# Optimization experiments

Measured on AMD Instinct MI355X. Metric: run time of the kernel, lower is better.

## Reference

```python
import jax, jax.numpy as jnp
import numpy as np

TAU = 2.0      # spikingjelly LIFNode default tau
V_TH = 1.0     # default v_threshold
ALPHA = 4.0    # default surrogate.Sigmoid alpha
H, HL = 8, 2   # num_heads, local_heads

@jax.custom_vjp
def spike(u):
    # Heaviside: fire when membrane potential >= threshold (u = v - v_th)
    return (u >= 0.0).astype(u.dtype)

def _spike_fwd(u):
    return spike(u), u

def _spike_bwd(u, g):
    s = jax.nn.sigmoid(ALPHA * u)
    return (g * ALPHA * s * (1.0 - s),)

spike.defvjp(_spike_fwd, _spike_bwd)

def lif(x):
    # Multi-step LIF, decay_input=False, v_reset=0.0 (hard reset), detach_reset=True.
    # Charge: v = v - (v - 0)/tau + x ; spike when v >= v_th ; reset v -> 0 where spiked.
    decay = 1.0 - 1.0 / TAU
    def step(v, xt):
        v = v * decay + xt
        s = spike(v - V_TH)
        v = v * (1.0 - jax.lax.stop_gradient(s))  # detach_reset
        return v, s
    _, spikes = jax.lax.scan(step, jnp.zeros_like(x[0]), x)
    return spikes

def setup_inputs() -> dict:
    key = jax.random.key(0)
    ks = jax.random.split(key, 5)
    T, B, C, D = 4, 8, 512, 768
    hd = D // H            # 96
    mkv = hd * HL          # 192 (GQA kv projection width)
    scale = 0.1            # keeps LIF membrane potentials near threshold
    return {
        "x": jax.random.normal(ks[0], (T, B, C, D), jnp.float32),
        "q_w": jax.random.normal(ks[1], (D, D), jnp.float32) * scale,
        "k_w": jax.random.normal(ks[2], (mkv, D), jnp.float32) * scale,
        "v_w": jax.random.normal(ks[3], (mkv, D), jnp.float32) * scale,
        "wo_w": jax.random.normal(ks[4], (D, D), jnp.float32) * scale,
    }

def reference(x, q_w, k_w, v_w, wo_w):
    T, B, C, D = x.shape
    hd = D // H
    n_rep = H // HL
    xs = lif(x)  # proj_lif
    # q: (T,B,C,D) -> (T,B,H,C,hd)
    q = lif(xs @ q_w.T).reshape(T, B, C, H, hd).transpose(0, 1, 3, 2, 4)
    # k,v: (T,B,C,mkv) -> repeat_interleave over kv heads -> (T,B,H,C,hd)
    k = lif(xs @ k_w.T).reshape(T, B, C, HL, hd)
    k = jnp.repeat(k, n_rep, axis=3).transpose(0, 1, 3, 2, 4)
    v = lif(xs @ v_w.T).reshape(T, B, C, HL, hd)
    v = jnp.repeat(v, n_rep, axis=3).transpose(0, 1, 3, 2, 4)
    # softmax-free attention: (q k^T) * 0.1 @ v
    scores = jnp.einsum('tbhqd,tbhkd->tbhqk', q, k) * 0.1
    out = jnp.einsum('tbhqk,tbhkd->tbhqd', scores, v)
    # (T,B,H,C,hd) -> (T,B,C,D)
    out = out.transpose(0, 1, 3, 2, 4).reshape(T, B, C, D)
    return out @ wo_w.T
```

## Files before the change

kernel.cpp:

```cpp
#include <hip/hip_runtime.h>

typedef __bf16 bf16;
typedef __bf16 bf16x8 __attribute__((ext_vector_type(8)));
typedef float f32x4 __attribute__((ext_vector_type(4)));

#define T_ 4
#define B_ 8
#define C_ 512
#define D_ 768
#define H_ 8
#define HL_ 2
#define HD_ 96
#define MKV_ 192
#define M2_ 4096
#define BCD_ 3145728
#define M3_ 16384
#define NCOMB 1152
#define SUSP_CAP 65536
#define SUSP_WIN 2e-4f

__device__ __forceinline__ void gld16(const bf16* g, bf16* l) {
    __builtin_amdgcn_global_load_lds(
        (const __attribute__((address_space(1))) unsigned int*)g,
        (__attribute__((address_space(3))) unsigned int*)l, 16, 0, 0);
}

__global__ __launch_bounds__(256) void prep_kernel(
    const float* __restrict__ x, const float* __restrict__ q_w,
    const float* __restrict__ k_w, const float* __restrict__ v_w,
    const float* __restrict__ wo_w, bf16* __restrict__ xs,
    bf16* __restrict__ whi, bf16* __restrict__ wlo, bf16* __restrict__ wo_bf,
    unsigned* __restrict__ susp)
{
    const int t0 = blockIdx.x * 256 + threadIdx.x;
    const int stride = gridDim.x * 256;
    if (t0 == 0) susp[0] = 0;
    for (int i = t0; i < BCD_; i += stride) {
        double v = 0.0;
        #pragma unroll
        for (int t = 0; t < T_; ++t) {
            v = v * 0.5 + (double)x[(size_t)t * BCD_ + i];
            float s = (v >= 1.0) ? 1.0f : 0.0f;
            xs[(size_t)t * BCD_ + i] = (bf16)s;
            if (s != 0.0f) v = 0.0;
        }
    }
    for (int i = t0; i < NCOMB * D_; i += stride) {
        int row = i / D_, col = i - row * D_;
        float v;
        if (row < 768)      v = q_w[(size_t)row * D_ + col];
        else if (row < 960) v = k_w[(size_t)(row - 768) * D_ + col];
        else                v = v_w[(size_t)(row - 960) * D_ + col];
        bf16 h = (bf16)v;
        whi[i] = h;
        wlo[i] = (bf16)(v - (float)h);
    }
    for (int i = t0; i < D_ * D_; i += stride)
        wo_bf[i] = (bf16)wo_w[i];
}

__global__ __launch_bounds__(256) void proj_lif_kernel(
    const bf16* __restrict__ xs, const bf16* __restrict__ Whi,
    const bf16* __restrict__ Wlo,
    bf16* __restrict__ q_sp, bf16* __restrict__ k_sp, bf16* __restrict__ v_sp,
    unsigned* __restrict__ susp)
{
    __shared__ __align__(16) bf16 Alds[T_][64 * 64];
    __shared__ __align__(16) bf16 Hlds[64 * 64];
    __shared__ __align__(16) bf16 Llds[64 * 64];

    const int tid  = threadIdx.x;
    const int wave = tid >> 6, lane = tid & 63;
    const int m16  = lane & 15, quad = lane >> 4;
    const int wm   = wave >> 1, wn = wave & 1;
    const int m0   = blockIdx.x * 64;
    const int n0   = blockIdx.y * 64;

    const int colb = n0 + wn * 32;
    bf16* outp; int Nloc, cb;
    if (colb < 768)      { outp = q_sp; Nloc = 768; cb = colb; }
    else if (colb < 960) { outp = k_sp; Nloc = 192; cb = colb - 768; }
    else                 { outp = v_sp; Nloc = 192; cb = colb - 960; }

    f32x4 acc[T_][2][2];
    #pragma unroll
    for (int t = 0; t < T_; t++)
        #pragma unroll
        for (int a = 0; a < 2; a++)
            #pragma unroll
            for (int b = 0; b < 2; b++) { f32x4 z = {0.f,0.f,0.f,0.f}; acc[t][a][b] = z; }

    for (int k0 = 0; k0 < D_; k0 += 64) {
        __syncthreads();
        #pragma unroll
        for (int j = 0; j < 8; j++) {
            int ci = j * 256 + tid;
            int t = ci >> 9, rem = ci & 511, row = rem >> 3, slot = rem & 7;
            int seg = slot ^ ((row >> 1) & 7);
            gld16(xs + (size_t)(t * M2_ + m0 + row) * D_ + k0 + seg * 8, &Alds[t][rem * 8]);
        }
        #pragma unroll
        for (int j = 0; j < 2; j++) {
            int ci = j * 256 + tid;
            int row = ci >> 3, slot = ci & 7;
            int seg = slot ^ ((row >> 1) & 7);
            gld16(Whi + (size_t)(n0 + row) * D_ + k0 + seg * 8, Hlds + ci * 8);
            gld16(Wlo + (size_t)(n0 + row) * D_ + k0 + seg * 8, Llds + ci * 8);
        }
        __syncthreads();

        #pragma unroll
        for (int kc = 0; kc < 2; kc++) {
            bf16x8 a[T_][2], bh[2], bl[2];
            #pragma unroll
            for (int mi = 0; mi < 2; mi++) {
                int row = wm * 32 + mi * 16 + m16;
                int off = row * 64 + (((kc * 4 + quad) ^ ((row >> 1) & 7)) * 8);
                #pragma unroll
                for (int t = 0; t < T_; t++)
                    a[t][mi] = *(const bf16x8*)&Alds[t][off];
            }
            #pragma unroll
            for (int ni = 0; ni < 2; ni++) {
                int row = wn * 32 + ni * 16 + m16;
                int off = row * 64 + (((kc * 4 + quad) ^ ((row >> 1) & 7)) * 8);
                bh[ni] = *(const bf16x8*)&Hlds[off];
                bl[ni] = *(const bf16x8*)&Llds[off];
            }
            #pragma unroll
            for (int ni = 0; ni < 2; ni++)
                #pragma unroll
                for (int t = 0; t < T_; t++)
                    #pragma unroll
                    for (int mi = 0; mi < 2; mi++) {
                        acc[t][mi][ni] = __builtin_amdgcn_mfma_f32_16x16x32_bf16(a[t][mi], bh[ni], acc[t][mi][ni], 0, 0, 0);
                        acc[t][mi][ni] = __builtin_amdgcn_mfma_f32_16x16x32_bf16(a[t][mi], bl[ni], acc[t][mi][ni], 0, 0, 0);
                    }
        }
    }

    #pragma unroll
    for (int mi = 0; mi < 2; mi++)
        #pragma unroll
        for (int ni = 0; ni < 2; ni++)
            #pragma unroll
            for (int rr = 0; rr < 4; rr++) {
                int row = m0 + wm * 32 + mi * 16 + quad * 4 + rr;
                int lc  = cb + ni * 16 + m16;
                float v = 0.f;
                bool suspect = false;
                #pragma unroll
                for (int t = 0; t < T_; t++) {
                    v = v * 0.5f + acc[t][mi][ni][rr];
                    float d = v - 1.0f;
                    if (fabsf(d) < SUSP_WIN) suspect = true;
                    float sp = (d >= 0.f) ? 1.f : 0.f;
                    v *= (1.f - sp);
                    outp[(size_t)(t * M2_ + row) * Nloc + lc] = (bf16)sp;
                }
                if (suspect) {
                    int ccol = n0 + wn * 32 + ni * 16 + m16;
                    unsigned idx = atomicAdd(susp, 1u);
                    if (idx < SUSP_CAP) susp[1 + idx] = (unsigned)(row * 2048 + ccol);
                }
            }
}

__global__ __launch_bounds__(256) void fixup_kernel(
    const bf16* __restrict__ xs, const float* __restrict__ q_w,
    const float* __restrict__ k_w, const float* __restrict__ v_w,
    bf16* __restrict__ q_sp, bf16* __restrict__ k_sp, bf16* __restrict__ v_sp,
    const unsigned* __restrict__ susp)
{
    unsigned count = susp[0];
    if (count > SUSP_CAP) count = SUSP_CAP;
    const int lane = threadIdx.x & 63;
    const int wid  = (blockIdx.x * blockDim.x + threadIdx.x) >> 6;
    const int nw   = (gridDim.x * blockDim.x) >> 6;
    for (unsigned i = wid; i < count; i += nw) {
        unsigned e = susp[1 + i];
        int row = e >> 11, col = e & 2047;
        const float* W; bf16* outp; int Nloc, lc;
        if (col < 768)      { W = q_w + (size_t)col * D_;         outp = q_sp; Nloc = 768; lc = col; }
        else if (col < 960) { W = k_w + (size_t)(col - 768) * D_; outp = k_sp; Nloc = 192; lc = col - 768; }
        else                { W = v_w + (size_t)(col - 960) * D_; outp = v_sp; Nloc = 192; lc = col - 960; }
        double v = 0.0;
        for (int t = 0; t < T_; ++t) {
            const bf16* ar = xs + (size_t)(t * M2_ + row) * D_;
            double y = 0.0;
            for (int k = lane; k < D_; k += 64)
                y += (double)(float)ar[k] * (double)W[k];
            #pragma unroll
            for (int off = 1; off < 64; off <<= 1)
                y += __shfl_xor(y, off);
            v = v * 0.5 + y;
            unsigned sp = (v >= 1.0) ? 1u : 0u;
            if (lane == 0) outp[(size_t)(t * M2_ + row) * Nloc + lc] = (bf16)(float)sp;
            if (sp) v = 0.0;
        }
    }
}

__global__ __launch_bounds__(256) void ktv_kernel(
    const bf16* __restrict__ k_sp, const bf16* __restrict__ v_sp,
    float* __restrict__ M_part)
{
    const int g    = blockIdx.x;
    const int cc   = blockIdx.y;
    const int kvh  = g % HL_;
    const int tb   = g / HL_;
    const int wave = threadIdx.x >> 6;
    const int lane = threadIdx.x & 63;
    const int m16  = lane & 15, quad = lane >> 4;

    __shared__ __align__(16) bf16 klds[96 * 40];
    __shared__ __align__(16) bf16 vlds[96 * 40];

    f32x4 acc[9];
    #pragma unroll
    for (int i = 0; i < 9; i++) { f32x4 z = {0.f,0.f,0.f,0.f}; acc[i] = z; }

    const bf16* kbase = k_sp + ((size_t)tb * C_ + cc * 128) * MKV_ + kvh * HD_;
    const bf16* vbase = v_sp + ((size_t)tb * C_ + cc * 128) * MKV_ + kvh * HD_;

    for (int c0 = 0; c0 < 128; c0 += 32) {
        __syncthreads();
        for (int idx = threadIdx.x; idx < 32 * 96; idx += 256) {
            int d = idx % 96;
            int c = idx / 96;
            klds[d * 40 + c] = kbase[(size_t)(c0 + c) * MKV_ + d];
            vlds[d * 40 + c] = vbase[(size_t)(c0 + c) * MKV_ + d];
        }
        __syncthreads();
        #pragma unroll
        for (int i = 0; i < 9; i++) {
            int tile = wave + i * 4;
            int mt = tile / 6, nt = tile % 6;
            bf16x8 a = *(const bf16x8*)(&klds[(mt * 16 + m16) * 40 + quad * 8]);
            bf16x8 b = *(const bf16x8*)(&vlds[(nt * 16 + m16) * 40 + quad * 8]);
            acc[i] = __builtin_amdgcn_mfma_f32_16x16x32_bf16(a, b, acc[i], 0, 0, 0);
        }
    }
    float* op = M_part + ((size_t)cc * 64 + g) * HD_ * HD_;
    #pragma unroll
    for (int i = 0; i < 9; i++) {
        int tile = wave + i * 4;
        int mt = tile / 6, nt = tile % 6;
        #pragma unroll
        for (int r = 0; r < 4; r++) {
            int d = mt * 16 + quad * 4 + r;
            int j = nt * 16 + m16;
            op[(size_t)j * HD_ + d] = acc[i][r];
        }
    }
}

__global__ __launch_bounds__(256) void cvtM_kernel(
    const float* __restrict__ M_part, bf16* __restrict__ M_hi,
    bf16* __restrict__ M_lo)
{
    int i = blockIdx.x * 256 + threadIdx.x;
    if (i >= 64 * HD_ * HD_) return;
    float m = M_part[i] + M_part[i + 589824] + M_part[i + 2 * 589824] + M_part[i + 3 * 589824];
    bf16 h = (bf16)m;
    M_hi[i] = h;
    M_lo[i] = (bf16)(m - (float)h);
}

__global__ __launch_bounds__(256) void qm_kernel(
    const bf16* __restrict__ q_sp, const bf16* __restrict__ M_hi,
    const bf16* __restrict__ M_lo, bf16* __restrict__ out_attn)
{
    const int tbh  = blockIdx.x;
    const int h    = tbh % H_;
    const int tb   = tbh / H_;
    const int g    = tb * HL_ + (h >> 2);
    const int wave = threadIdx.x >> 6;
    const int lane = threadIdx.x & 63;
    const int m16  = lane & 15, quad = lane >> 4;
    const int cw   = blockIdx.y * 128 + wave * 32;

    __shared__ __align__(16) bf16 Mh[96 * 104];
    __shared__ __align__(16) bf16 Ml[96 * 104];
    {
        const bf16* gh = M_hi + (size_t)g * HD_ * HD_;
        const bf16* gl = M_lo + (size_t)g * HD_ * HD_;
        #pragma unroll
        for (int j = 0; j < 5; j++) {
            int ci = j * 256 + threadIdx.x;
            if (ci < 1152) {
                int row = ci / 12, seg = ci % 12;
                *(bf16x8*)&Mh[row * 104 + seg * 8] = *(const bf16x8*)(gh + row * HD_ + seg * 8);
                *(bf16x8*)&Ml[row * 104 + seg * 8] = *(const bf16x8*)(gl + row * HD_ + seg * 8);
            }
        }
    }
    __syncthreads();

    f32x4 acc[2][6];
    #pragma unroll
    for (int mi = 0; mi < 2; mi++)
        #pragma unroll
        for (int nt = 0; nt < 6; nt++) { f32x4 z = {0.f,0.f,0.f,0.f}; acc[mi][nt] = z; }

    #pragma unroll
    for (int ks = 0; ks < 3; ++ks) {
        bf16x8 a[2];
        #pragma unroll
        for (int mi = 0; mi < 2; mi++)
            a[mi] = *(const bf16x8*)(q_sp + ((size_t)(tb * C_ + cw + mi * 16 + m16)) * D_
                                     + h * HD_ + ks * 32 + quad * 8);
        #pragma unroll
        for (int nt = 0; nt < 6; ++nt) {
            bf16x8 bh = *(const bf16x8*)&Mh[(nt * 16 + m16) * 104 + ks * 32 + quad * 8];
            bf16x8 bl = *(const bf16x8*)&Ml[(nt * 16 + m16) * 104 + ks * 32 + quad * 8];
            #pragma unroll
            for (int mi = 0; mi < 2; mi++) {
                acc[mi][nt] = __builtin_amdgcn_mfma_f32_16x16x32_bf16(a[mi], bh, acc[mi][nt], 0, 0, 0);
                acc[mi][nt] = __builtin_amdgcn_mfma_f32_16x16x32_bf16(a[mi], bl, acc[mi][nt], 0, 0, 0);
            }
        }
    }
    #pragma unroll
    for (int mi = 0; mi < 2; mi++)
        #pragma unroll
        for (int nt = 0; nt < 6; nt++)
            #pragma unroll
            for (int r = 0; r < 4; r++) {
                int c = cw + mi * 16 + quad * 4 + r;
                int j = nt * 16 + m16;
                out_attn[((size_t)(tb * C_ + c)) * D_ + h * HD_ + j] = (bf16)(0.1f * acc[mi][nt][r]);
            }
}

__global__ __launch_bounds__(256) void final_gemm_kernel(
    const bf16* __restrict__ A, const bf16* __restrict__ W, float* __restrict__ out)
{
    __shared__ __align__(16) bf16 Alds[128 * 64];
    __shared__ __align__(16) bf16 Blds[128 * 64];
    const int tid  = threadIdx.x;
    const int wave = tid >> 6, lane = tid & 63;
    const int m16  = lane & 15, quad = lane >> 4;
    const int wm   = wave >> 1, wn = wave & 1;
    const int m0   = blockIdx.x * 128, n0 = blockIdx.y * 128;

    f32x4 acc[4][4];
    #pragma unroll
    for (int a = 0; a < 4; a++)
        #pragma unroll
        for (int b = 0; b < 4; b++) { f32x4 z = {0.f,0.f,0.f,0.f}; acc[a][b] = z; }

    for (int k0 = 0; k0 < D_; k0 += 64) {
        __syncthreads();
        #pragma unroll
        for (int j = 0; j < 4; j++) {
            int ci = j * 256 + tid;
            int row = ci >> 3, slot = ci & 7;
            int seg = slot ^ ((row >> 1) & 7);
            gld16(A + (size_t)(m0 + row) * D_ + k0 + seg * 8, Alds + ci * 8);
            gld16(W + (size_t)(n0 + row) * D_ + k0 + seg * 8, Blds + ci * 8);
        }
        __syncthreads();
        #pragma unroll
        for (int kc = 0; kc < 2; kc++) {
            bf16x8 a[4], b[4];
            #pragma unroll
            for (int mi = 0; mi < 4; mi++) {
                int row = wm * 64 + mi * 16 + m16;
                a[mi] = *(const bf16x8*)&Alds[row * 64 + (((kc * 4 + quad) ^ ((row >> 1) & 7)) * 8)];
            }
            #pragma unroll
            for (int ni = 0; ni < 4; ni++) {
                int row = wn * 64 + ni * 16 + m16;
                b[ni] = *(const bf16x8*)&Blds[row * 64 + (((kc * 4 + quad) ^ ((row >> 1) & 7)) * 8)];
            }
            #pragma unroll
            for (int mi = 0; mi < 4; mi++)
                #pragma unroll
                for (int ni = 0; ni < 4; ni++)
                    acc[mi][ni] = __builtin_amdgcn_mfma_f32_16x16x32_bf16(a[mi], b[ni], acc[mi][ni], 0, 0, 0);
        }
    }
    #pragma unroll
    for (int mi = 0; mi < 4; mi++)
        #pragma unroll
        for (int ni = 0; ni < 4; ni++)
            #pragma unroll
            for (int r = 0; r < 4; r++) {
                int row = m0 + wm * 64 + mi * 16 + quad * 4 + r;
                int col = n0 + wn * 64 + ni * 16 + m16;
                out[(size_t)row * D_ + col] = acc[mi][ni][r];
            }
}

extern "C" void kernel_launch(void* const* d_in, const int* in_sizes, int n_in,
                              void* d_out, int out_size, void* d_ws, size_t ws_size,
                              hipStream_t stream) {
    const float* x    = (const float*)d_in[0];
    const float* q_w  = (const float*)d_in[1];
    const float* k_w  = (const float*)d_in[2];
    const float* v_w  = (const float*)d_in[3];
    const float* wo_w = (const float*)d_in[4];
    float* out = (float*)d_out;

    char* ws = (char*)d_ws;
    bf16* xs    = (bf16*)(ws);
    bf16* q_sp  = (bf16*)(ws + 25165824);
    bf16* k_sp  = (bf16*)(ws + 50331648);
    bf16* v_sp  = (bf16*)(ws + 56623104);
    bf16* whi   = (bf16*)(ws + 62914560);
    bf16* wlo   = (bf16*)(ws + 64684032);
    bf16* wo_bf = (bf16*)(ws + 66453504);
    bf16* M_hi  = (bf16*)(ws + 67633152);
    bf16* M_lo  = (bf16*)(ws + 68812800);
    unsigned* susp = (unsigned*)(ws + 69992448);
    bf16* out_attn = xs;
    float* M_part  = out;

    hipLaunchKernelGGL(prep_kernel, dim3(2048), dim3(256), 0, stream,
                       x, q_w, k_w, v_w, wo_w, xs, whi, wlo, wo_bf, susp);
    hipLaunchKernelGGL(proj_lif_kernel, dim3(M2_ / 64, NCOMB / 64), dim3(256), 0, stream,
                       xs, whi, wlo, q_sp, k_sp, v_sp, susp);
    hipLaunchKernelGGL(fixup_kernel, dim3(256), dim3(256), 0, stream,
                       xs, q_w, k_w, v_w, q_sp, k_sp, v_sp, susp);
    hipLaunchKernelGGL(ktv_kernel, dim3(T_ * B_ * HL_, 4), dim3(256), 0, stream,
                       k_sp, v_sp, M_part);
    hipLaunchKernelGGL(cvtM_kernel, dim3((64 * HD_ * HD_ + 255) / 256), dim3(256), 0, stream,
                       M_part, M_hi, M_lo);
    hipLaunchKernelGGL(qm_kernel, dim3(T_ * B_ * H_, C_ / 128), dim3(256), 0, stream,
                       q_sp, M_hi, M_lo, out_attn);
    hipLaunchKernelGGL(final_gemm_kernel, dim3(M3_ / 128, D_ / 128), dim3(256), 0, stream,
                       out_attn, wo_bf, out);
}
```

Before: 279.6 us.

## Fuse suspect fixup into projection, atomically reduce KtV, drop conversion kernel

Several changes land together. The fp64 recheck of near-threshold LIF outputs now runs inside the projection kernel through a per-wave ballot, which removes the separate fixup launch and the global atomic suspect list. The projection tile widens to 128 columns with launch_bounds(256,2). KtV partials are accumulated into a zeroed fp32 buffer with atomicAdd, and the hi/lo bf16 split moves into qm_kernel's LDS load, which removes cvtM_kernel. The KtV LDS staging is also vectorized with an XOR swizzle. The costs are fp32 atomic contention, nondeterministic summation order, higher register pressure, and serialized fp64 fixup work within waves.

```diff
diff --git a/kernel.cpp b/kernel.cpp
--- a/kernel.cpp
+++ b/kernel.cpp
@@ -16,7 +16,6 @@
 #define BCD_ 3145728
 #define M3_ 16384
 #define NCOMB 1152
-#define SUSP_CAP 65536
 #define SUSP_WIN 2e-4f
 
 __device__ __forceinline__ void gld16(const bf16* g, bf16* l) {
@@ -30,11 +29,10 @@
     const float* __restrict__ k_w, const float* __restrict__ v_w,
     const float* __restrict__ wo_w, bf16* __restrict__ xs,
     bf16* __restrict__ whi, bf16* __restrict__ wlo, bf16* __restrict__ wo_bf,
-    unsigned* __restrict__ susp)
+    float* __restrict__ M_f32)
 {
     const int t0 = blockIdx.x * 256 + threadIdx.x;
     const int stride = gridDim.x * 256;
-    if (t0 == 0) susp[0] = 0;
     for (int i = t0; i < BCD_; i += stride) {
         double v = 0.0;
         #pragma unroll
@@ -57,38 +55,41 @@
     }
     for (int i = t0; i < D_ * D_; i += stride)
         wo_bf[i] = (bf16)wo_w[i];
-}
-
-__global__ __launch_bounds__(256) void proj_lif_kernel(
+    for (int i = t0; i < 64 * HD_ * HD_; i += stride)
+        M_f32[i] = 0.f;
+}
+
+__global__ __launch_bounds__(256, 2) void proj_lif_kernel(
     const bf16* __restrict__ xs, const bf16* __restrict__ Whi,
     const bf16* __restrict__ Wlo,
-    bf16* __restrict__ q_sp, bf16* __restrict__ k_sp, bf16* __restrict__ v_sp,
-    unsigned* __restrict__ susp)
+    const float* __restrict__ q_w, const float* __restrict__ k_w,
+    const float* __restrict__ v_w,
+    bf16* __restrict__ q_sp, bf16* __restrict__ k_sp, bf16* __restrict__ v_sp)
 {
     __shared__ __align__(16) bf16 Alds[T_][64 * 64];
-    __shared__ __align__(16) bf16 Hlds[64 * 64];
-    __shared__ __align__(16) bf16 Llds[64 * 64];
+    __shared__ __align__(16) bf16 Hlds[128 * 64];
+    __shared__ __align__(16) bf16 Llds[128 * 64];
 
     const int tid  = threadIdx.x;
     const int wave = tid >> 6, lane = tid & 63;
     const int m16  = lane & 15, quad = lane >> 4;
     const int wm   = wave >> 1, wn = wave & 1;
     const int m0   = blockIdx.x * 64;
-    const int n0   = blockIdx.y * 64;
-
-    const int colb = n0 + wn * 32;
+    const int n0   = blockIdx.y * 128;
+
+    const int colb = n0 + wn * 64;
     bf16* outp; int Nloc, cb;
     if (colb < 768)      { outp = q_sp; Nloc = 768; cb = colb; }
     else if (colb < 960) { outp = k_sp; Nloc = 192; cb = colb - 768; }
     else                 { outp = v_sp; Nloc = 192; cb = colb - 960; }
 
-    f32x4 acc[T_][2][2];
+    f32x4 acc[T_][2][4];
     #pragma unroll
     for (int t = 0; t < T_; t++)
         #pragma unroll
         for (int a = 0; a < 2; a++)
             #pragma unroll
-            for (int b = 0; b < 2; b++) { f32x4 z = {0.f,0.f,0.f,0.f}; acc[t][a][b] = z; }
+            for (int b = 0; b < 4; b++) { f32x4 z = {0.f,0.f,0.f,0.f}; acc[t][a][b] = z; }
 
     for (int k0 = 0; k0 < D_; k0 += 64) {
         __syncthreads();
@@ -100,7 +101,7 @@
             gld16(xs + (size_t)(t * M2_ + m0 + row) * D_ + k0 + seg * 8, &Alds[t][rem * 8]);
         }
         #pragma unroll
-        for (int j = 0; j < 2; j++) {
+        for (int j = 0; j < 4; j++) {
             int ci = j * 256 + tid;
             int row = ci >> 3, slot = ci & 7;
             int seg = slot ^ ((row >> 1) & 7);
@@ -111,7 +112,7 @@
 
         #pragma unroll
         for (int kc = 0; kc < 2; kc++) {
-            bf16x8 a[T_][2], bh[2], bl[2];
+            bf16x8 a[T_][2], bh[4], bl[4];
             #pragma unroll
             for (int mi = 0; mi < 2; mi++) {
                 int row = wm * 32 + mi * 16 + m16;
@@ -121,14 +122,14 @@
                     a[t][mi] = *(const bf16x8*)&Alds[t][off];
             }
             #pragma unroll
-            for (int ni = 0; ni < 2; ni++) {
-                int row = wn * 32 + ni * 16 + m16;
+            for (int ni = 0; ni < 4; ni++) {
+                int row = wn * 64 + ni * 16 + m16;
                 int off = row * 64 + (((kc * 4 + quad) ^ ((row >> 1) & 7)) * 8);
                 bh[ni] = *(const bf16x8*)&Hlds[off];
                 bl[ni] = *(const bf16x8*)&Llds[off];
             }
             #pragma unroll
-            for (int ni = 0; ni < 2; ni++)
+            for (int ni = 0; ni < 4; ni++)
                 #pragma unroll
                 for (int t = 0; t < T_; t++)
                     #pragma unroll
@@ -139,16 +140,18 @@
         }
     }
 
+    unsigned suspectBits = 0;
     #pragma unroll
     for (int mi = 0; mi < 2; mi++)
         #pragma unroll
-        for (int ni = 0; ni < 2; ni++)
+        for (int ni = 0; ni < 4; ni++)
             #pragma unroll
             for (int rr = 0; rr < 4; rr++) {
                 int row = m0 + wm * 32 + mi * 16 + quad * 4 + rr;
                 int lc  = cb + ni * 16 + m16;
                 float v = 0.f;
                 bool suspect = false;
+                float spk[T_];
                 #pragma unroll
                 for (int t = 0; t < T_; t++) {
                     v = v * 0.5f + acc[t][mi][ni][rr];
@@ -156,54 +159,50 @@
                     if (fabsf(d) < SUSP_WIN) suspect = true;
                     float sp = (d >= 0.f) ? 1.f : 0.f;
                     v *= (1.f - sp);
-                    outp[(size_t)(t * M2_ + row) * Nloc + lc] = (bf16)sp;
+                    spk[t] = sp;
                 }
-                if (suspect) {
-                    int ccol = n0 + wn * 32 + ni * 16 + m16;
-                    unsigned idx = atomicAdd(susp, 1u);
-                    if (idx < SUSP_CAP) susp[1 + idx] = (unsigned)(row * 2048 + ccol);
+                if (!suspect) {
+                    #pragma unroll
+                    for (int t = 0; t < T_; t++)
+                        outp[(size_t)(t * M2_ + row) * Nloc + lc] = (bf16)spk[t];
+                } else {
+                    suspectBits |= 1u << (mi * 16 + ni * 4 + rr);
                 }
             }
-}
-
-__global__ __launch_bounds__(256) void fixup_kernel(
-    const bf16* __restrict__ xs, const float* __restrict__ q_w,
-    const float* __restrict__ k_w, const float* __restrict__ v_w,
-    bf16* __restrict__ q_sp, bf16* __restrict__ k_sp, bf16* __restrict__ v_sp,
-    const unsigned* __restrict__ susp)
-{
-    unsigned count = susp[0];
-    if (count > SUSP_CAP) count = SUSP_CAP;
-    const int lane = threadIdx.x & 63;
-    const int wid  = (blockIdx.x * blockDim.x + threadIdx.x) >> 6;
-    const int nw   = (gridDim.x * blockDim.x) >> 6;
-    for (unsigned i = wid; i < count; i += nw) {
-        unsigned e = susp[1 + i];
-        int row = e >> 11, col = e & 2047;
-        const float* W; bf16* outp; int Nloc, lc;
-        if (col < 768)      { W = q_w + (size_t)col * D_;         outp = q_sp; Nloc = 768; lc = col; }
-        else if (col < 960) { W = k_w + (size_t)(col - 768) * D_; outp = k_sp; Nloc = 192; lc = col - 768; }
-        else                { W = v_w + (size_t)(col - 960) * D_; outp = v_sp; Nloc = 192; lc = col - 960; }
-        double v = 0.0;
-        for (int t = 0; t < T_; ++t) {
-            const bf16* ar = xs + (size_t)(t * M2_ + row) * D_;
-            double y = 0.0;
-            for (int k = lane; k < D_; k += 64)
-                y += (double)(float)ar[k] * (double)W[k];
-            #pragma unroll
-            for (int off = 1; off < 64; off <<= 1)
-                y += __shfl_xor(y, off);
-            v = v * 0.5 + y;
-            unsigned sp = (v >= 1.0) ? 1u : 0u;
-            if (lane == 0) outp[(size_t)(t * M2_ + row) * Nloc + lc] = (bf16)(float)sp;
-            if (sp) v = 0.0;
+
+    for (int slot = 0; slot < 32; ++slot) {
+        unsigned long long mask = __ballot((suspectBits >> slot) & 1u);
+        while (mask) {
+            int l = __ffsll((long long)mask) - 1;
+            mask &= mask - 1;
+            int mi = slot >> 4, ni = (slot >> 2) & 3, rr = slot & 3;
+            int row  = m0 + wm * 32 + mi * 16 + (l >> 4) * 4 + rr;
+            int gcol = n0 + wn * 64 + ni * 16 + (l & 15);
+            const float* W; bf16* op; int Nl, lc;
+            if (gcol < 768)      { W = q_w + (size_t)gcol * D_;         op = q_sp; Nl = 768; lc = gcol; }
+            else if (gcol < 960) { W = k_w + (size_t)(gcol - 768) * D_; op = k_sp; Nl = 192; lc = gcol - 768; }
+            else                 { W = v_w + (size_t)(gcol - 960) * D_; op = v_sp; Nl = 192; lc = gcol - 960; }
+            double v = 0.0;
+            for (int t = 0; t < T_; ++t) {
+                const bf16* ar = xs + (size_t)(t * M2_ + row) * D_;
+                double y = 0.0;
+                for (int k = lane; k < D_; k += 64)
+                    y += (double)(float)ar[k] * (double)W[k];
+                #pragma unroll
+                for (int off = 1; off < 64; off <<= 1)
+                    y += __shfl_xor(y, off);
+                v = v * 0.5 + y;
+                unsigned sp = (v >= 1.0) ? 1u : 0u;
+                if (lane == 0) op[(size_t)(t * M2_ + row) * Nl + lc] = (bf16)(float)sp;
+                if (sp) v = 0.0;
+            }
         }
     }
 }
 
 __global__ __launch_bounds__(256) void ktv_kernel(
     const bf16* __restrict__ k_sp, const bf16* __restrict__ v_sp,
-    float* __restrict__ M_part)
+    float* __restrict__ M_f32)
 {
     const int g    = blockIdx.x;
     const int cc   = blockIdx.y;
@@ -225,23 +224,34 @@
 
     for (int c0 = 0; c0 < 128; c0 += 32) {
         __syncthreads();
-        for (int idx = threadIdx.x; idx < 32 * 96; idx += 256) {
-            int d = idx % 96;
-            int c = idx / 96;
-            klds[d * 40 + c] = kbase[(size_t)(c0 + c) * MKV_ + d];
-            vlds[d * 40 + c] = vbase[(size_t)(c0 + c) * MKV_ + d];
+        #pragma unroll
+        for (int jj = 0; jj < 2; jj++) {
+            int ci = jj * 256 + threadIdx.x;
+            if (ci < 384) {
+                int c = ci / 12, seg = ci - (ci / 12) * 12;
+                bf16x8 kv = *(const bf16x8*)(kbase + (size_t)(c0 + c) * MKV_ + seg * 8);
+                bf16x8 vv = *(const bf16x8*)(vbase + (size_t)(c0 + c) * MKV_ + seg * 8);
+                int cs = c ^ ((seg & 3) << 3);
+                #pragma unroll
+                for (int j = 0; j < 8; j++) {
+                    int d = seg * 8 + j;
+                    klds[d * 40 + cs] = kv[j];
+                    vlds[d * 40 + cs] = vv[j];
+                }
+            }
         }
         __syncthreads();
         #pragma unroll
         for (int i = 0; i < 9; i++) {
             int tile = wave + i * 4;
             int mt = tile / 6, nt = tile % 6;
-            bf16x8 a = *(const bf16x8*)(&klds[(mt * 16 + m16) * 40 + quad * 8]);
-            bf16x8 b = *(const bf16x8*)(&vlds[(nt * 16 + m16) * 40 + quad * 8]);
+            int rowA = mt * 16 + m16, rowB = nt * 16 + m16;
+            bf16x8 a = *(const bf16x8*)&klds[rowA * 40 + ((quad * 8) ^ (((rowA >> 3) & 3) << 3))];
+            bf16x8 b = *(const bf16x8*)&vlds[rowB * 40 + ((quad * 8) ^ (((rowB >> 3) & 3) << 3))];
             acc[i] = __builtin_amdgcn_mfma_f32_16x16x32_bf16(a, b, acc[i], 0, 0, 0);
         }
     }
-    float* op = M_part + ((size_t)cc * 64 + g) * HD_ * HD_;
+    float* op = M_f32 + (size_t)g * HD_ * HD_;
     #pragma unroll
     for (int i = 0; i < 9; i++) {
         int tile = wave + i * 4;
@@ -250,26 +260,14 @@
         for (int r = 0; r < 4; r++) {
             int d = mt * 16 + quad * 4 + r;
             int j = nt * 16 + m16;
-            op[(size_t)j * HD_ + d] = acc[i][r];
-        }
-    }
-}
-
-__global__ __launch_bounds__(256) void cvtM_kernel(
-    const float* __restrict__ M_part, bf16* __restrict__ M_hi,
-    bf16* __restrict__ M_lo)
-{
-    int i = blockIdx.x * 256 + threadIdx.x;
-    if (i >= 64 * HD_ * HD_) return;
-    float m = M_part[i] + M_part[i + 589824] + M_part[i + 2 * 589824] + M_part[i + 3 * 589824];
-    bf16 h = (bf16)m;
-    M_hi[i] = h;
-    M_lo[i] = (bf16)(m - (float)h);
+            atomicAdd(&op[(size_t)j * HD_ + d], acc[i][r]);
+        }
+    }
 }
 
 __global__ __launch_bounds__(256) void qm_kernel(
-    const bf16* __restrict__ q_sp, const bf16* __restrict__ M_hi,
-    const bf16* __restrict__ M_lo, bf16* __restrict__ out_attn)
+    const bf16* __restrict__ q_sp, const float* __restrict__ M_f32,
+    bf16* __restrict__ out_attn)
 {
     const int tbh  = blockIdx.x;
     const int h    = tbh % H_;
@@ -283,15 +281,20 @@
     __shared__ __align__(16) bf16 Mh[96 * 104];
     __shared__ __align__(16) bf16 Ml[96 * 104];
     {
-        const bf16* gh = M_hi + (size_t)g * HD_ * HD_;
-        const bf16* gl = M_lo + (size_t)g * HD_ * HD_;
-        #pragma unroll
-        for (int j = 0; j < 5; j++) {
+        const float* Mg = M_f32 + (size_t)g * HD_ * HD_;
+        #pragma unroll
+        for (int j = 0; j < 9; j++) {
             int ci = j * 256 + threadIdx.x;
-            if (ci < 1152) {
-                int row = ci / 12, seg = ci % 12;
-                *(bf16x8*)&Mh[row * 104 + seg * 8] = *(const bf16x8*)(gh + row * HD_ + seg * 8);
-                *(bf16x8*)&Ml[row * 104 + seg * 8] = *(const bf16x8*)(gl + row * HD_ + seg * 8);
+            if (ci < 2304) {
+                f32x4 m4 = *(const f32x4*)(Mg + ci * 4);
+                int e = ci * 4, row = e / 96, colj = e - row * 96;
+                #pragma unroll
+                for (int xx = 0; xx < 4; xx++) {
+                    float m = m4[xx];
+                    bf16 hh = (bf16)m;
+                    Mh[row * 104 + colj + xx] = hh;
+                    Ml[row * 104 + colj + xx] = (bf16)(m - (float)hh);
+                }
             }
         }
     }
@@ -411,24 +414,17 @@
     bf16* whi   = (bf16*)(ws + 62914560);
     bf16* wlo   = (bf16*)(ws + 64684032);
     bf16* wo_bf = (bf16*)(ws + 66453504);
-    bf16* M_hi  = (bf16*)(ws + 67633152);
-    bf16* M_lo  = (bf16*)(ws + 68812800);
-    unsigned* susp = (unsigned*)(ws + 69992448);
+    float* M_f32 = (float*)(ws + 67633152);
     bf16* out_attn = xs;
-    float* M_part  = out;
 
     hipLaunchKernelGGL(prep_kernel, dim3(2048), dim3(256), 0, stream,
-                       x, q_w, k_w, v_w, wo_w, xs, whi, wlo, wo_bf, susp);
-    hipLaunchKernelGGL(proj_lif_kernel, dim3(M2_ / 64, NCOMB / 64), dim3(256), 0, stream,
-                       xs, whi, wlo, q_sp, k_sp, v_sp, susp);
-    hipLaunchKernelGGL(fixup_kernel, dim3(256), dim3(256), 0, stream,
-                       xs, q_w, k_w, v_w, q_sp, k_sp, v_sp, susp);
+                       x, q_w, k_w, v_w, wo_w, xs, whi, wlo, wo_bf, M_f32);
+    hipLaunchKernelGGL(proj_lif_kernel, dim3(M2_ / 64, NCOMB / 128), dim3(256), 0, stream,
+                       xs, whi, wlo, q_w, k_w, v_w, q_sp, k_sp, v_sp);
     hipLaunchKernelGGL(ktv_kernel, dim3(T_ * B_ * HL_, 4), dim3(256), 0, stream,
-                       k_sp, v_sp, M_part);
-    hipLaunchKernelGGL(cvtM_kernel, dim3((64 * HD_ * HD_ + 255) / 256), dim3(256), 0, stream,
-                       M_part, M_hi, M_lo);
+                       k_sp, v_sp, M_f32);
     hipLaunchKernelGGL(qm_kernel, dim3(T_ * B_ * H_, C_ / 128), dim3(256), 0, stream,
-                       q_sp, M_hi, M_lo, out_attn);
+                       q_sp, M_f32, out_attn);
     hipLaunchKernelGGL(final_gemm_kernel, dim3(M3_ / 128, D_ / 128), dim3(256), 0, stream,
                        out_attn, wo_bf, out);
 }
```

Result: slower. 295.8 us (+5.8%).
